# Kernel optimization log

Measured on AMD Instinct MI355X. Metric: run time of the kernel, lower is better.

The kernel has to match this reference:

```python
import jax, jax.numpy as jnp
import numpy as np

TEMPERATURE = 2.0


def _off_diag(x):
    # Equivalent to torch masked_select((1-eye).bool()).view(n, n-1): drop the
    # diagonal of an (n, n) matrix in row-major order -> (n, n-1).
    n = x.shape[0]
    return x.reshape(-1)[:-1].reshape(n - 1, n + 1)[:, 1:].reshape(n, n - 1)


def setup_inputs() -> dict:
    key = jax.random.key(0)
    k1, k2, k3 = jax.random.split(key, 3)
    B, D, L = 2048, 256, 1
    z1 = jax.random.normal(k1, (B, D), dtype=jnp.float32)
    z2 = jax.random.normal(k2, (B, D), dtype=jnp.float32)
    labels = jax.random.uniform(k3, (B, L), dtype=jnp.float32)
    return {"z1": z1, "z2": z2, "labels": labels}


def reference(z1, z2, labels):
    t = TEMPERATURE
    feats = jnp.concatenate([z1, z2], axis=0)          # (n, d)
    lab = jnp.tile(labels, (2, 1))                     # (n, L), labels.repeat(2,1)
    n = feats.shape[0]

    # L1 label differences: |l_i - l_j| summed over label dims -> (n, n)
    label_diffs = jnp.abs(lab[:, None, :] - lab[None, :, :]).sum(axis=-1)

    # Negative L2 feature similarity via the sq-norm expansion (avoids (n,n,d)).
    r = jnp.sum(feats * feats, axis=-1)                # (n,)
    sq = jnp.maximum(r[:, None] + r[None, :] - 2.0 * (feats @ feats.T), 0.0)
    # Diagonal is removed from the loss below; set it to 1 so sqrt is grad-safe.
    sq = jnp.where(jnp.eye(n, dtype=bool), 1.0, sq)
    logits = -jnp.sqrt(sq) / t                          # (n, n)

    # Detached row-max subtraction (pure numerical shift; cancels in log-probs).
    logits = logits - jax.lax.stop_gradient(jnp.max(logits, axis=1, keepdims=True))

    lo = _off_diag(logits)                              # (n, n-1)
    ex = jnp.exp(lo)                                    # (n, n-1)
    ld = _off_diag(label_diffs)                         # (n, n-1)

    # The torch loop computes, for each anchor i and positive k:
    #   denom[i,k] = sum_j ex[i,j] * (ld[i,j] >= ld[i,k])
    # Exact O(n^2 log n) form: sort each row by label diff, suffix-cumsum the
    # exponentials, and start the suffix at the FIRST occurrence of each value
    # (searchsorted 'left') so ties are included exactly as '>=' does.
    order = jnp.argsort(ld, axis=-1)
    ld_s = jnp.take_along_axis(ld, order, axis=-1)
    ex_s = jnp.take_along_axis(ex, order, axis=-1)
    lo_s = jnp.take_along_axis(lo, order, axis=-1)
    suffix = jnp.cumsum(ex_s[:, ::-1], axis=-1)[:, ::-1]      # suffix sums
    start = jax.vmap(lambda a, v: jnp.searchsorted(a, v, side="left"))(ld_s, ld_s)
    denom = jnp.take_along_axis(suffix, start, axis=-1)        # (n, n-1)

    # Sum over (i, k) is permutation-invariant, so sum in sorted order.
    log_probs = lo_s - jnp.log(denom)
    loss = -jnp.sum(log_probs) / (n * (n - 1))
    return loss
```

## Files before the change

kernel.cpp:

```cpp
#include <hip/hip_runtime.h>
#include <hip/hip_bf16.h>

#define NROWS 4096
#define NLAB  2048
#define NPAIR 2048
#define FMAXV 3.402823466e+38f

typedef __attribute__((ext_vector_type(8))) short short8;
typedef __attribute__((ext_vector_type(8))) unsigned short ushort8;
typedef __attribute__((ext_vector_type(4))) float f32x4;

__device__ __forceinline__ unsigned short f2bf(float x) {
  unsigned int u = __float_as_uint(x);
  unsigned int r = u + 0x7fffu + ((u >> 16) & 1u);
  return (unsigned short)(r >> 16);
}
__device__ __forceinline__ float bf2f(unsigned short h) {
  return __uint_as_float(((unsigned int)h) << 16);
}

__global__ __launch_bounds__(256) void prep_kernel(const float* __restrict__ labels,
                                                   const float* __restrict__ z1,
                                                   const float* __restrict__ z2,
                                                   unsigned short* __restrict__ Fb,
                                                   float* __restrict__ rs,
                                                   float* __restrict__ ssorted2,
                                                   int* __restrict__ pl2v) {
  __shared__ float L[NLAB];
  const int tid = threadIdx.x;
  const int lane = tid & 63, wid = tid >> 6;
  for (int t = tid; t < NLAB; t += 256) L[t] = labels[t];
  __syncthreads();
  const int i = blockIdx.x * 4 + wid;
  const float a = L[i & (NLAB - 1)];
  int combo = 0;
  #pragma unroll 4
  for (int jj = 0; jj < NLAB / 64; ++jj) {
    const int j = jj * 64 + lane;
    const float l = L[j];
    if (l < a) combo += 2 + (2 << 13);
    else if (l == a) combo += ((j < i) + (j + NLAB < i)) + (2 << 13);
  }
  #pragma unroll
  for (int off = 32; off > 0; off >>= 1) combo += __shfl_down(combo, off, 64);
  combo = __shfl(combo, 0, 64);
  const int cnt = combo & 8191, cle = combo >> 13;
  const float* src = (i < NLAB) ? (z1 + (size_t)i * 256)
                                : (z2 + (size_t)(i - NLAB) * 256);
  float4 v = ((const float4*)src)[lane];
  ushort4 o;
  o.x = f2bf(v.x); o.y = f2bf(v.y); o.z = f2bf(v.z); o.w = f2bf(v.w);
  ((ushort4*)Fb)[(size_t)cnt * 64 + lane] = o;
  float ss = v.x * v.x + v.y * v.y + v.z * v.z + v.w * v.w;
  #pragma unroll
  for (int off = 32; off > 0; off >>= 1) ss += __shfl_down(ss, off, 64);
  if (lane == 0) {
    rs[cnt] = ss;
    if (!(cnt & 1)) {
      ssorted2[cnt >> 1] = a;
      pl2v[cnt >> 1] = (cle >> 1) - 1;
    }
  }
}

__global__ __launch_bounds__(256) void gemm_kernel(const unsigned short* __restrict__ Fb,
                                                   unsigned short* __restrict__ Gslab,
                                                   int row0) {
  __shared__ unsigned short tile[64][66];
  const int tid = threadIdx.x;
  const int lane = tid & 63, wid = tid >> 6;
  const int wm = wid >> 1, wn = wid & 1;
  const int m0 = row0 + blockIdx.x * 64 + wm * 32;
  const int n0 = blockIdx.y * 64 + wn * 32;
  const int r16 = lane & 15, kg = lane >> 4;
  const f32x4 z = {0.f, 0.f, 0.f, 0.f};
  f32x4 acc00 = z, acc01 = z, acc10 = z, acc11 = z;
  const unsigned short* pa0 = Fb + (size_t)(m0 + r16) * 256 + kg * 8;
  const unsigned short* pa1 = pa0 + 16 * 256;
  const unsigned short* pb0 = Fb + (size_t)(n0 + r16) * 256 + kg * 8;
  const unsigned short* pb1 = pb0 + 16 * 256;
  #pragma unroll
  for (int ks = 0; ks < 8; ++ks) {
    const int k0 = ks * 32;
    short8 a0 = *(const short8*)(pa0 + k0);
    short8 a1 = *(const short8*)(pa1 + k0);
    short8 b0 = *(const short8*)(pb0 + k0);
    short8 b1 = *(const short8*)(pb1 + k0);
    acc00 = __builtin_amdgcn_mfma_f32_16x16x32_bf16(a0, b0, acc00, 0, 0, 0);
    acc01 = __builtin_amdgcn_mfma_f32_16x16x32_bf16(a0, b1, acc01, 0, 0, 0);
    acc10 = __builtin_amdgcn_mfma_f32_16x16x32_bf16(a1, b0, acc10, 0, 0, 0);
    acc11 = __builtin_amdgcn_mfma_f32_16x16x32_bf16(a1, b1, acc11, 0, 0, 0);
  }
  const int lr = wm * 32 + kg * 4, lc = wn * 32 + r16;
  #pragma unroll
  for (int rr = 0; rr < 4; ++rr) {
    tile[lr + rr][lc]           = f2bf(acc00[rr]);
    tile[lr + rr][lc + 16]      = f2bf(acc01[rr]);
    tile[lr + 16 + rr][lc]      = f2bf(acc10[rr]);
    tile[lr + 16 + rr][lc + 16] = f2bf(acc11[rr]);
  }
  __syncthreads();
  const int lm = blockIdx.x * 64;
  const int gcol = blockIdx.y * 64 + (tid & 7) * 8;
  #pragma unroll
  for (int k = 0; k < 2; ++k) {
    const int row = k * 32 + (tid >> 3);
    ushort8 v = *(const ushort8*)&tile[row][(tid & 7) * 8];
    *(ushort8*)(Gslab + (size_t)(lm + row) * NROWS + gcol) = v;
  }
}

__global__ __launch_bounds__(512, 8) void main_kernel(const unsigned short* __restrict__ G,
                                                      const float* __restrict__ rs,
                                                      const float* __restrict__ ssorted2,
                                                      const int* __restrict__ pl2v,
                                                      int pair0, float2* __restrict__ part) {
  __shared__ float s2[NPAIR];
  __shared__ float2 P2[NPAIR];
  __shared__ float2 wsum[8];
  __shared__ float4 red[8];
  const int tid = threadIdx.x;
  const int jj = pair0 + blockIdx.x;
  const int mA = 2 * jj, mB = mA + 1;
  *(float4*)&s2[tid * 4] = ((const float4*)ssorted2)[tid];
  const float a = ssorted2[jj];
  const float ra = rs[mA], rb = rs[mB];
  const int pL2 = pl2v[jj];
  float loA = 0.f, loB = 0.f;
  float wA0, wA1, wA2, wA3, wA4, wA5, wA6, wA7;
  float wB0, wB1, wB2, wB3, wB4, wB5, wB6, wB7;
  {
    const ushort8 gva = ((const ushort8*)(G + (size_t)(2 * blockIdx.x) * NROWS))[tid];
    const ushort8 gvb = ((const ushort8*)(G + (size_t)(2 * blockIdx.x + 1) * NROWS))[tid];
    const float4 rt0 = ((const float4*)rs)[tid * 2];
    const float4 rt1 = ((const float4*)rs)[tid * 2 + 1];
    const int t = tid * 8;
    #define DOW(U, RT, WA, WB) { \
      WA = 0.f; WB = 0.f; \
      if (t + U != mA) { \
        float lo = -0.5f * __builtin_amdgcn_sqrtf(fmaxf(ra + RT - 2.f * bf2f(gva[U]), 0.f)); \
        loA += lo; WA = __expf(lo); } \
      if (t + U != mB) { \
        float lo = -0.5f * __builtin_amdgcn_sqrtf(fmaxf(rb + RT - 2.f * bf2f(gvb[U]), 0.f)); \
        loB += lo; WB = __expf(lo); } }
    DOW(0, rt0.x, wA0, wB0) DOW(1, rt0.y, wA1, wB1)
    DOW(2, rt0.z, wA2, wB2) DOW(3, rt0.w, wA3, wB3)
    DOW(4, rt1.x, wA4, wB4) DOW(5, rt1.y, wA5, wB5)
    DOW(6, rt1.z, wA6, wB6) DOW(7, rt1.w, wA7, wB7)
    #undef DOW
  }
  const float ca0 = wA0 + wA1, cb0 = wB0 + wB1;
  const float ca1 = ca0 + wA2 + wA3, cb1 = cb0 + wB2 + wB3;
  const float ca2 = ca1 + wA4 + wA5, cb2 = cb1 + wB4 + wB5;
  const float ca3 = ca2 + wA6 + wA7, cb3 = cb2 + wB6 + wB7;
  const int lane = tid & 63, wid = tid >> 6;
  float xa = ca3, xb = cb3;
  #pragma unroll
  for (int off = 1; off < 64; off <<= 1) {
    float ya = __shfl_up(xa, off, 64);
    float yb = __shfl_up(xb, off, 64);
    if (lane >= off) { xa += ya; xb += yb; }
  }
  if (lane == 63) wsum[wid] = make_float2(xa, xb);
  __syncthreads();
  float woffA = 0.f, woffB = 0.f, PtotA = 0.f, PtotB = 0.f;
  #pragma unroll
  for (int w = 0; w < 8; ++w) {
    float2 ws = wsum[w];
    PtotA += ws.x; PtotB += ws.y;
    if (w < wid) { woffA += ws.x; woffB += ws.y; }
  }
  const float exclA = woffA + xa - ca3, exclB = woffB + xb - cb3;
  const float PA0 = exclA + ca0, PA1 = exclA + ca1, PA2 = exclA + ca2, PA3 = exclA + ca3;
  const float PB0 = exclB + cb0, PB1 = exclB + cb1, PB2 = exclB + cb2, PB3 = exclB + cb3;
  const int pb = tid * 4;
  ((float4*)P2)[tid * 2]     = make_float4(PA0, PB0, PA1, PB1);
  ((float4*)P2)[tid * 2 + 1] = make_float4(PA2, PB2, PA3, PB3);
  __syncthreads();
  const float4 s2o = *(const float4*)&s2[pb];
  int rR = -1;
  int qL = -1; bool qInit = false;
  float prodA = 1.f, prodB = 1.f;
  #define STEP(U, SV, INCA, INCB, PRVA, PRVB) { \
    const int p = pb + U; \
    float WA, WB; \
    if (p <= pL2) { \
      const float v = a - SV; \
      if (rR < 0) { int lo = pL2 + 1, hi = NPAIR; \
        while (lo < hi) { int m = (lo + hi) >> 1; \
          if (s2[m] - a >= v) hi = m; else lo = m + 1; } rR = lo; } \
      else { while (rR > pL2 + 1 && s2[rR - 1] - a >= v) --rR; } \
      const float2 Pq = P2[rR - 1]; \
      WA = Pq.x - INCA; WB = Pq.y - INCB; \
    } else { \
      const float v = SV - a; \
      if (!qInit) { int lo = 0, hi = pL2 + 1; \
        while (lo < hi) { int m = (lo + hi) >> 1; \
          if (a - s2[m] >= v) lo = m + 1; else hi = m; } qL = lo - 1; qInit = true; } \
      else { while (qL >= 0 && a - s2[qL] < v) --qL; } \
      const float2 Pq = (qL >= 0) ? P2[qL] : make_float2(0.f, 0.f); \
      WA = PRVA - Pq.x; WB = PRVB - Pq.y; \
    } \
    prodA *= (PtotA - WA); prodB *= (PtotB - WB); }
  STEP(0, s2o.x, PA0, PB0, exclA, exclB)
  STEP(1, s2o.y, PA1, PB1, PA0, PB0)
  STEP(2, s2o.z, PA2, PB2, PA1, PB1)
  STEP(3, s2o.w, PA3, PB3, PA2, PB2)
  #undef STEP
  float ldA = __logf(prodA), ldB = __logf(prodB);
  #pragma unroll
  for (int off = 32; off > 0; off >>= 1) {
    loA += __shfl_down(loA, off, 64);
    loB += __shfl_down(loB, off, 64);
    ldA += __shfl_down(ldA, off, 64);
    ldB += __shfl_down(ldB, off, 64);
  }
  if (lane == 0) red[wid] = make_float4(loA, ldA, loB, ldB);
  __syncthreads();
  if (tid == 0) {
    float LA = 0.f, DA = 0.f, LB = 0.f, DB = 0.f;
    #pragma unroll
    for (int w = 0; w < 8; ++w) {
      float4 q = red[w];
      LA += q.x; DA += q.y; LB += q.z; DB += q.w;
    }
    part[mA] = make_float2(LA, 2.f * DA - __logf(PtotA));
    part[mB] = make_float2(LB, 2.f * DB - __logf(PtotB));
  }
}

__global__ __launch_bounds__(512) void final_kernel(const float2* __restrict__ part,
                                                    float* __restrict__ out) {
  const int tid = threadIdx.x;
  double L = 0.0, D = 0.0;
  for (int t = tid; t < NROWS; t += 512) {
    float2 p = part[t];
    L += (double)p.x; D += (double)p.y;
  }
  const int lane = tid & 63, wid = tid >> 6;
  #pragma unroll
  for (int off = 32; off > 0; off >>= 1) {
    L += __shfl_down(L, off, 64);
    D += __shfl_down(D, off, 64);
  }
  __shared__ double sL[8], sD[8];
  if (lane == 0) { sL[wid] = L; sD[wid] = D; }
  __syncthreads();
  if (tid == 0) {
    double Ls = 0.0, Ds = 0.0;
    #pragma unroll
    for (int w = 0; w < 8; ++w) { Ls += sL[w]; Ds += sD[w]; }
    out[0] = (float)((Ds - Ls) / 16773120.0);
  }
}

extern "C" void kernel_launch(void* const* d_in, const int* in_sizes, int n_in,
                              void* d_out, int out_size, void* d_ws, size_t ws_size,
                              hipStream_t stream) {
  (void)in_sizes; (void)n_in; (void)out_size;
  const float* z1     = (const float*)d_in[0];
  const float* z2     = (const float*)d_in[1];
  const float* labels = (const float*)d_in[2];
  float* out = (float*)d_out;

  char* ws = (char*)d_ws;
  float2* part           = (float2*)ws;
  float*  ssorted2       = (float*)(ws + 32768);
  float*  rs             = (float*)(ws + 40960);
  int*    pl2v           = (int*)(ws + 57344);
  unsigned short* Fb     = (unsigned short*)(ws + 131072);
  const size_t G_off = (size_t)4 << 20;
  unsigned short* G = (unsigned short*)(ws + G_off);

  size_t pairs_cap = (ws_size > G_off + (size_t)64 * 16384)
                         ? (ws_size - G_off) / 16384 : 64;
  int R2 = (int)((pairs_cap / 64) * 64);
  if (R2 < 64) R2 = 64;
  if (R2 > NLAB) R2 = NLAB;

  prep_kernel<<<1024, 256, 0, stream>>>(labels, z1, z2, Fb, rs, ssorted2, pl2v);
  for (int p0 = 0; p0 < NLAB; p0 += R2) {
    int pairs = NLAB - p0; if (pairs > R2) pairs = R2;
    gemm_kernel<<<dim3(pairs * 2 / 64, NROWS / 64), 256, 0, stream>>>(Fb, G, 2 * p0);
    main_kernel<<<pairs, 512, 0, stream>>>(G, rs, ssorted2, pl2v, p0, part);
  }
  final_kernel<<<1, 512, 0, stream>>>(part, out);
}
```

Measured before the change: 157.8 us.

## Fuse Gram GEMM into per-row loss kernel, keeping similarities in LDS

Replaces the separate bf16 GEMM, which wrote the Gram matrix to global memory, and the per-pair main kernel with a single fused kernel. Each block owns 16 rows and computes their Gram columns with MFMA, converts them to exponentials and pair sums in padded shared memory, then prefix-scans and runs the label-sorted denominator search per row. This removes the global round trip of the Gram matrix and one kernel launch. In exchange only 256 blocks run with large LDS use and one block per CU. The search loop is also serialized over 64 elements per lane, and the fp32 accumulator is no longer rounded to bf16.

Result: slower. 220.4 us (+39.7%).

```diff
diff --git a/kernel.cpp b/kernel.cpp
--- a/kernel.cpp
+++ b/kernel.cpp
@@ -4,19 +4,16 @@
 #define NROWS 4096
 #define NLAB  2048
 #define NPAIR 2048
-#define FMAXV 3.402823466e+38f
+#define PADW  2052
+#define SIDX(p) ((p) + ((p) >> 5))
 
 typedef __attribute__((ext_vector_type(8))) short short8;
-typedef __attribute__((ext_vector_type(8))) unsigned short ushort8;
 typedef __attribute__((ext_vector_type(4))) float f32x4;
 
 __device__ __forceinline__ unsigned short f2bf(float x) {
   unsigned int u = __float_as_uint(x);
   unsigned int r = u + 0x7fffu + ((u >> 16) & 1u);
   return (unsigned short)(r >> 16);
-}
-__device__ __forceinline__ float bf2f(unsigned short h) {
-  return __uint_as_float(((unsigned int)h) << 16);
 }
 
 __global__ __launch_bounds__(256) void prep_kernel(const float* __restrict__ labels,
@@ -63,169 +60,128 @@
   }
 }
 
-__global__ __launch_bounds__(256) void gemm_kernel(const unsigned short* __restrict__ Fb,
-                                                   unsigned short* __restrict__ Gslab,
-                                                   int row0) {
-  __shared__ unsigned short tile[64][66];
+__global__ __launch_bounds__(512, 1) void fused_kernel(const unsigned short* __restrict__ Fb,
+                                                       const float* __restrict__ rs,
+                                                       const float* __restrict__ ssorted2,
+                                                       const int* __restrict__ pl2v,
+                                                       float2* __restrict__ part) {
+  __shared__ float s2s[NPAIR + NPAIR / 32];
+  __shared__ float P2[16 * PADW];
+  __shared__ float lab16[16];
+  __shared__ int   pl16[16];
+  __shared__ float losr[8][16];
+  __shared__ float Ptot16[16];
+  __shared__ float ld16[16];
   const int tid = threadIdx.x;
-  const int lane = tid & 63, wid = tid >> 6;
-  const int wm = wid >> 1, wn = wid & 1;
-  const int m0 = row0 + blockIdx.x * 64 + wm * 32;
-  const int n0 = blockIdx.y * 64 + wn * 32;
+  const int lane = tid & 63, w = tid >> 6;
   const int r16 = lane & 15, kg = lane >> 4;
-  const f32x4 z = {0.f, 0.f, 0.f, 0.f};
-  f32x4 acc00 = z, acc01 = z, acc10 = z, acc11 = z;
-  const unsigned short* pa0 = Fb + (size_t)(m0 + r16) * 256 + kg * 8;
-  const unsigned short* pa1 = pa0 + 16 * 256;
-  const unsigned short* pb0 = Fb + (size_t)(n0 + r16) * 256 + kg * 8;
-  const unsigned short* pb1 = pb0 + 16 * 256;
-  #pragma unroll
-  for (int ks = 0; ks < 8; ++ks) {
-    const int k0 = ks * 32;
-    short8 a0 = *(const short8*)(pa0 + k0);
-    short8 a1 = *(const short8*)(pa1 + k0);
-    short8 b0 = *(const short8*)(pb0 + k0);
-    short8 b1 = *(const short8*)(pb1 + k0);
-    acc00 = __builtin_amdgcn_mfma_f32_16x16x32_bf16(a0, b0, acc00, 0, 0, 0);
-    acc01 = __builtin_amdgcn_mfma_f32_16x16x32_bf16(a0, b1, acc01, 0, 0, 0);
-    acc10 = __builtin_amdgcn_mfma_f32_16x16x32_bf16(a1, b0, acc10, 0, 0, 0);
-    acc11 = __builtin_amdgcn_mfma_f32_16x16x32_bf16(a1, b1, acc11, 0, 0, 0);
-  }
-  const int lr = wm * 32 + kg * 4, lc = wn * 32 + r16;
-  #pragma unroll
-  for (int rr = 0; rr < 4; ++rr) {
-    tile[lr + rr][lc]           = f2bf(acc00[rr]);
-    tile[lr + rr][lc + 16]      = f2bf(acc01[rr]);
-    tile[lr + 16 + rr][lc]      = f2bf(acc10[rr]);
-    tile[lr + 16 + rr][lc + 16] = f2bf(acc11[rr]);
-  }
-  __syncthreads();
-  const int lm = blockIdx.x * 64;
-  const int gcol = blockIdx.y * 64 + (tid & 7) * 8;
-  #pragma unroll
-  for (int k = 0; k < 2; ++k) {
-    const int row = k * 32 + (tid >> 3);
-    ushort8 v = *(const ushort8*)&tile[row][(tid & 7) * 8];
-    *(ushort8*)(Gslab + (size_t)(lm + row) * NROWS + gcol) = v;
-  }
-}
-
-__global__ __launch_bounds__(512, 8) void main_kernel(const unsigned short* __restrict__ G,
-                                                      const float* __restrict__ rs,
-                                                      const float* __restrict__ ssorted2,
-                                                      const int* __restrict__ pl2v,
-                                                      int pair0, float2* __restrict__ part) {
-  __shared__ float s2[NPAIR];
-  __shared__ float2 P2[NPAIR];
-  __shared__ float2 wsum[8];
-  __shared__ float4 red[8];
-  const int tid = threadIdx.x;
-  const int jj = pair0 + blockIdx.x;
-  const int mA = 2 * jj, mB = mA + 1;
-  *(float4*)&s2[tid * 4] = ((const float4*)ssorted2)[tid];
-  const float a = ssorted2[jj];
-  const float ra = rs[mA], rb = rs[mB];
-  const int pL2 = pl2v[jj];
-  float loA = 0.f, loB = 0.f;
-  float wA0, wA1, wA2, wA3, wA4, wA5, wA6, wA7;
-  float wB0, wB1, wB2, wB3, wB4, wB5, wB6, wB7;
+  const int rowbase = blockIdx.x * 16;
   {
-    const ushort8 gva = ((const ushort8*)(G + (size_t)(2 * blockIdx.x) * NROWS))[tid];
-    const ushort8 gvb = ((const ushort8*)(G + (size_t)(2 * blockIdx.x + 1) * NROWS))[tid];
-    const float4 rt0 = ((const float4*)rs)[tid * 2];
-    const float4 rt1 = ((const float4*)rs)[tid * 2 + 1];
-    const int t = tid * 8;
-    #define DOW(U, RT, WA, WB) { \
-      WA = 0.f; WB = 0.f; \
-      if (t + U != mA) { \
-        float lo = -0.5f * __builtin_amdgcn_sqrtf(fmaxf(ra + RT - 2.f * bf2f(gva[U]), 0.f)); \
-        loA += lo; WA = __expf(lo); } \
-      if (t + U != mB) { \
-        float lo = -0.5f * __builtin_amdgcn_sqrtf(fmaxf(rb + RT - 2.f * bf2f(gvb[U]), 0.f)); \
-        loB += lo; WB = __expf(lo); } }
-    DOW(0, rt0.x, wA0, wB0) DOW(1, rt0.y, wA1, wB1)
-    DOW(2, rt0.z, wA2, wB2) DOW(3, rt0.w, wA3, wB3)
-    DOW(4, rt1.x, wA4, wB4) DOW(5, rt1.y, wA5, wB5)
-    DOW(6, rt1.z, wA6, wB6) DOW(7, rt1.w, wA7, wB7)
-    #undef DOW
-  }
-  const float ca0 = wA0 + wA1, cb0 = wB0 + wB1;
-  const float ca1 = ca0 + wA2 + wA3, cb1 = cb0 + wB2 + wB3;
-  const float ca2 = ca1 + wA4 + wA5, cb2 = cb1 + wB4 + wB5;
-  const float ca3 = ca2 + wA6 + wA7, cb3 = cb2 + wB6 + wB7;
-  const int lane = tid & 63, wid = tid >> 6;
-  float xa = ca3, xb = cb3;
-  #pragma unroll
-  for (int off = 1; off < 64; off <<= 1) {
-    float ya = __shfl_up(xa, off, 64);
-    float yb = __shfl_up(xb, off, 64);
-    if (lane >= off) { xa += ya; xb += yb; }
-  }
-  if (lane == 63) wsum[wid] = make_float2(xa, xb);
-  __syncthreads();
-  float woffA = 0.f, woffB = 0.f, PtotA = 0.f, PtotB = 0.f;
-  #pragma unroll
-  for (int w = 0; w < 8; ++w) {
-    float2 ws = wsum[w];
-    PtotA += ws.x; PtotB += ws.y;
-    if (w < wid) { woffA += ws.x; woffB += ws.y; }
-  }
-  const float exclA = woffA + xa - ca3, exclB = woffB + xb - cb3;
-  const float PA0 = exclA + ca0, PA1 = exclA + ca1, PA2 = exclA + ca2, PA3 = exclA + ca3;
-  const float PB0 = exclB + cb0, PB1 = exclB + cb1, PB2 = exclB + cb2, PB3 = exclB + cb3;
-  const int pb = tid * 4;
-  ((float4*)P2)[tid * 2]     = make_float4(PA0, PB0, PA1, PB1);
-  ((float4*)P2)[tid * 2 + 1] = make_float4(PA2, PB2, PA3, PB3);
-  __syncthreads();
-  const float4 s2o = *(const float4*)&s2[pb];
-  int rR = -1;
-  int qL = -1; bool qInit = false;
-  float prodA = 1.f, prodB = 1.f;
-  #define STEP(U, SV, INCA, INCB, PRVA, PRVB) { \
-    const int p = pb + U; \
-    float WA, WB; \
-    if (p <= pL2) { \
-      const float v = a - SV; \
-      if (rR < 0) { int lo = pL2 + 1, hi = NPAIR; \
-        while (lo < hi) { int m = (lo + hi) >> 1; \
-          if (s2[m] - a >= v) hi = m; else lo = m + 1; } rR = lo; } \
-      else { while (rR > pL2 + 1 && s2[rR - 1] - a >= v) --rR; } \
-      const float2 Pq = P2[rR - 1]; \
-      WA = Pq.x - INCA; WB = Pq.y - INCB; \
-    } else { \
-      const float v = SV - a; \
-      if (!qInit) { int lo = 0, hi = pL2 + 1; \
-        while (lo < hi) { int m = (lo + hi) >> 1; \
-          if (a - s2[m] >= v) lo = m + 1; else hi = m; } qL = lo - 1; qInit = true; } \
-      else { while (qL >= 0 && a - s2[qL] < v) --qL; } \
-      const float2 Pq = (qL >= 0) ? P2[qL] : make_float2(0.f, 0.f); \
-      WA = PRVA - Pq.x; WB = PRVB - Pq.y; \
-    } \
-    prodA *= (PtotA - WA); prodB *= (PtotB - WB); }
-  STEP(0, s2o.x, PA0, PB0, exclA, exclB)
-  STEP(1, s2o.y, PA1, PB1, PA0, PB0)
-  STEP(2, s2o.z, PA2, PB2, PA1, PB1)
-  STEP(3, s2o.w, PA3, PB3, PA2, PB2)
-  #undef STEP
-  float ldA = __logf(prodA), ldB = __logf(prodB);
-  #pragma unroll
-  for (int off = 32; off > 0; off >>= 1) {
-    loA += __shfl_down(loA, off, 64);
-    loB += __shfl_down(loB, off, 64);
-    ldA += __shfl_down(ldA, off, 64);
-    ldB += __shfl_down(ldB, off, 64);
-  }
-  if (lane == 0) red[wid] = make_float4(loA, ldA, loB, ldB);
-  __syncthreads();
-  if (tid == 0) {
-    float LA = 0.f, DA = 0.f, LB = 0.f, DB = 0.f;
-    #pragma unroll
-    for (int w = 0; w < 8; ++w) {
-      float4 q = red[w];
-      LA += q.x; DA += q.y; LB += q.z; DB += q.w;
-    }
-    part[mA] = make_float2(LA, 2.f * DA - __logf(PtotA));
-    part[mB] = make_float2(LB, 2.f * DB - __logf(PtotB));
+    const float4 v = ((const float4*)ssorted2)[tid];
+    const int p = tid * 4;
+    s2s[SIDX(p)] = v.x; s2s[SIDX(p) + 1] = v.y;
+    s2s[SIDX(p) + 2] = v.z; s2s[SIDX(p) + 3] = v.w;
+    if (tid < 16) {
+      lab16[tid] = ssorted2[(rowbase + tid) >> 1];
+      pl16[tid]  = pl2v[(rowbase + tid) >> 1];
+    }
+  }
+  const int R = rowbase + r16;
+  const float ra = rs[R];
+  short8 bfr[8];
+  {
+    const unsigned short* pb = Fb + (size_t)R * 256 + kg * 8;
+    #pragma unroll
+    for (int ks = 0; ks < 8; ++ks) bfr[ks] = *(const short8*)(pb + ks * 32);
+  }
+  float losum = 0.f;
+  #pragma unroll 1
+  for (int it = 0; it < 32; ++it) {
+    const int tb = (w + it * 8) * 16;
+    const unsigned short* pa = Fb + (size_t)(tb + r16) * 256 + kg * 8;
+    f32x4 acc = {0.f, 0.f, 0.f, 0.f};
+    #pragma unroll
+    for (int ks = 0; ks < 8; ++ks)
+      acc = __builtin_amdgcn_mfma_f32_16x16x32_bf16(*(const short8*)(pa + ks * 32),
+                                                    bfr[ks], acc, 0, 0, 0);
+    const float4 rc = *(const float4*)(rs + tb + kg * 4);
+    const float rcv[4] = {rc.x, rc.y, rc.z, rc.w};
+    float wv[4];
+    #pragma unroll
+    for (int rr = 0; rr < 4; ++rr) {
+      const int c = tb + kg * 4 + rr;
+      const float sq = fmaxf(ra + rcv[rr] - 2.f * acc[rr], 0.f);
+      float lo = -0.5f * __builtin_amdgcn_sqrtf(sq);
+      const bool self = (c == R);
+      lo = self ? 0.f : lo;
+      losum += lo;
+      wv[rr] = self ? 0.f : __expf(lo);
+    }
+    const int cp0 = (tb >> 1) + kg * 2;
+    *(float2*)&P2[r16 * PADW + cp0] = make_float2(wv[0] + wv[1], wv[2] + wv[3]);
+  }
+  losum += __shfl_down(losum, 32, 64);
+  losum += __shfl_down(losum, 16, 64);
+  if (lane < 16) losr[w][lane] = losum;
+  __syncthreads();
+  const int half = lane >> 5, lh = lane & 31;
+  const int r2 = 2 * w + half;
+  float* __restrict__ Prow = &P2[r2 * PADW];
+  float carry = 0.f;
+  #pragma unroll
+  for (int c = 0; c < 16; ++c) {
+    const int cp = c * 128 + lh * 4;
+    const float4 v = *(const float4*)&Prow[cp];
+    const float t0 = v.x, t1 = t0 + v.y, t2 = t1 + v.z, t3 = t2 + v.w;
+    float x = t3;
+    #pragma unroll
+    for (int off = 1; off < 32; off <<= 1) {
+      const float y = __shfl_up(x, off, 32);
+      if (lh >= off) x += y;
+    }
+    const float base = carry + x - t3;
+    *(float4*)&Prow[cp] = make_float4(base + t0, base + t1, base + t2, base + t3);
+    carry += __shfl(x, 31, 32);
+  }
+  const float Ptot = carry;
+  if (lh == 0) Ptot16[r2] = Ptot;
+  const float a2 = lab16[r2];
+  const int pL2 = pl16[r2];
+  const int p0 = lh * 64;
+  int rR = -1, qL = -1; bool qInit = false;
+  float logden = 0.f, prod = 1.f; int pm = 0;
+  #pragma unroll 1
+  for (int s = 0; s < 64; ++s) {
+    const int p = p0 + s;
+    const float sv = s2s[SIDX(p)];
+    float W;
+    if (p <= pL2) {
+      const float v = a2 - sv;
+      if (rR < 0) { int lo = pL2 + 1, hi = NPAIR;
+        while (lo < hi) { int m = (lo + hi) >> 1;
+          if (s2s[SIDX(m)] - a2 >= v) hi = m; else lo = m + 1; } rR = lo; }
+      else { while (rR > pL2 + 1 && s2s[SIDX(rR - 1)] - a2 >= v) --rR; }
+      W = Prow[rR - 1] - Prow[p];
+    } else {
+      const float v = sv - a2;
+      if (!qInit) { int lo = 0, hi = pL2 + 1;
+        while (lo < hi) { int m = (lo + hi) >> 1;
+          if (a2 - s2s[SIDX(m)] >= v) lo = m + 1; else hi = m; } qL = lo - 1; qInit = true; }
+      else { while (qL >= 0 && a2 - s2s[SIDX(qL)] < v) --qL; }
+      W = Prow[p - 1] - (qL >= 0 ? Prow[qL] : 0.f);
+    }
+    prod *= (Ptot - W);
+    if (++pm == 4) { logden += __logf(prod); prod = 1.f; pm = 0; }
+  }
+  #pragma unroll
+  for (int off = 16; off > 0; off >>= 1) logden += __shfl_down(logden, off, 32);
+  if (lh == 0) ld16[r2] = logden;
+  __syncthreads();
+  if (tid < 16) {
+    float L = 0.f;
+    #pragma unroll
+    for (int ww = 0; ww < 8; ++ww) L += losr[ww][tid];
+    part[rowbase + tid] = make_float2(L, 2.f * ld16[tid] - __logf(Ptot16[tid]));
   }
 }
 
@@ -257,7 +213,7 @@
 extern "C" void kernel_launch(void* const* d_in, const int* in_sizes, int n_in,
                               void* d_out, int out_size, void* d_ws, size_t ws_size,
                               hipStream_t stream) {
-  (void)in_sizes; (void)n_in; (void)out_size;
+  (void)in_sizes; (void)n_in; (void)out_size; (void)ws_size;
   const float* z1     = (const float*)d_in[0];
   const float* z2     = (const float*)d_in[1];
   const float* labels = (const float*)d_in[2];
@@ -269,20 +225,8 @@
   float*  rs             = (float*)(ws + 40960);
   int*    pl2v           = (int*)(ws + 57344);
   unsigned short* Fb     = (unsigned short*)(ws + 131072);
-  const size_t G_off = (size_t)4 << 20;
-  unsigned short* G = (unsigned short*)(ws + G_off);
-
-  size_t pairs_cap = (ws_size > G_off + (size_t)64 * 16384)
-                         ? (ws_size - G_off) / 16384 : 64;
-  int R2 = (int)((pairs_cap / 64) * 64);
-  if (R2 < 64) R2 = 64;
-  if (R2 > NLAB) R2 = NLAB;
 
   prep_kernel<<<1024, 256, 0, stream>>>(labels, z1, z2, Fb, rs, ssorted2, pl2v);
-  for (int p0 = 0; p0 < NLAB; p0 += R2) {
-    int pairs = NLAB - p0; if (pairs > R2) pairs = R2;
-    gemm_kernel<<<dim3(pairs * 2 / 64, NROWS / 64), 256, 0, stream>>>(Fb, G, 2 * p0);
-    main_kernel<<<pairs, 512, 0, stream>>>(G, rs, ssorted2, pl2v, p0, part);
-  }
+  fused_kernel<<<256, 512, 0, stream>>>(Fb, rs, ssorted2, pl2v, part);
   final_kernel<<<1, 512, 0, stream>>>(part, out);
 }
```
